# Performance work log

Hardware: AMD Instinct MI355X
Metric: run time of the kernel (lower is better)

The kernel has to match this reference:

```python
import jax, jax.numpy as jnp
import numpy as np

B, T, K = 32, 8192, 16
EPS = 1e-7
LAM_FIRE, LAM_CANCEL, LAM_VALID, LAM_WRITE = 1.0, 1.0, 0.5, 0.5


def setup_inputs() -> dict:
    key = jax.random.key(0)
    ks = jax.random.split(key, 11)
    return {
        "trigger_hazard": jax.random.uniform(ks[0], (B, T, K), jnp.float32),
        "validity": jax.random.uniform(ks[1], (B, T, K), jnp.float32),
        "cancel_logits": jax.random.normal(ks[2], (B, T, K, 3), jnp.float32),
        "write_score": jax.random.normal(ks[3], (B, T, 1), jnp.float32),
        "live_mask": jax.random.randint(ks[4], (B, T, K), 0, 2).astype(bool),
        "contract_id": jax.random.randint(ks[5], (B, T, K), 0, 32),
        "oracle_fire": jax.random.randint(ks[6], (B, T, K), 0, 2).astype(jnp.float32),
        "oracle_cancel": jax.random.randint(ks[7], (B, T, K), 0, 4),
        "oracle_valid": jax.random.randint(ks[8], (B, T, K), 0, 2).astype(jnp.float32),
        "oracle_should_write": jax.random.randint(ks[9], (B, T, 1), 0, 2).astype(jnp.float32),
        "oracle_contract_id": jax.random.randint(ks[10], (B, T, K), 0, 32),
    }


def _masked_bce(p_raw, y, m):
    # Mirrors torch: BCE(clamp(p)*mask, y*mask), then *mask, sum / clamp(mask.sum(),1)
    n = jnp.maximum(m.sum(), 1.0)
    p = jnp.clip(p_raw, EPS, 1.0 - EPS) * m
    t = y * m
    # extra inner clip only guards masked entries (p==0), which are zeroed anyway
    bce = -(t * jnp.log(jnp.clip(p, EPS)) + (1.0 - t) * jnp.log(jnp.clip(1.0 - p, EPS)))
    return (bce * m).sum() / n


def _cancel_ce(logits, cancel_tgt, live_mask):
    has = ((cancel_tgt > 0) & live_mask).astype(jnp.float32)  # (B,T,K)
    n = has.sum()
    tgt = jnp.clip(cancel_tgt - 1, 0).astype(jnp.int32)
    logp = jax.nn.log_softmax(logits, axis=-1)  # (B,T,K,3)
    ce = -jnp.take_along_axis(logp, tgt[..., None], axis=-1)[..., 0]
    return jnp.where(n > 0, (ce * has).sum() / jnp.maximum(n, 1.0), 0.0)


def _bce_with_logits(x, y):
    return jnp.mean(jnp.maximum(x, 0.0) - x * y + jnp.log1p(jnp.exp(-jnp.abs(x))))


def reference(trigger_hazard, validity, cancel_logits, write_score, live_mask,
              contract_id, oracle_fire, oracle_cancel, oracle_valid,
              oracle_should_write, oracle_contract_id):
    # Vectorized align_oracle_to_model: broadcast compare + first-match argmax + gather
    match = (contract_id[..., :, None] == oracle_contract_id[..., None, :]) \
            & (contract_id != 0)[..., None]              # (B,T,Km,Ko)
    found = match.any(axis=-1)                           # (B,T,Km)
    idx = jnp.argmax(match, axis=-1)                     # first matching oracle slot

    def align_f(x):  # float tensors -> zeros where unmatched (torch out = zeros float)
        return jnp.where(found, jnp.take_along_axis(x, idx, axis=2), 0.0)

    fire_t = align_f(oracle_fire)
    valid_t = align_f(oracle_valid)
    cancel_t = jnp.where(found, jnp.take_along_axis(oracle_cancel, idx, axis=2), 0)

    m = live_mask.astype(jnp.float32)
    fire = LAM_FIRE * _masked_bce(trigger_hazard, fire_t, m)
    cancel = LAM_CANCEL * _cancel_ce(cancel_logits, cancel_t, live_mask)
    valid = LAM_VALID * _masked_bce(validity, valid_t, m)
    write = LAM_WRITE * _bce_with_logits(write_score, oracle_should_write)
    total = fire + cancel + valid + write
    return jnp.stack([fire, cancel, valid, write, total])
```

## Files before the change

### kernel.cpp

```cpp
#include <hip/hip_runtime.h>
#include <math.h>

#define EPS_F 1e-7f

constexpr int Bc = 32, Tc = 8192, Kc = 16;
constexpr int ROWS  = Bc * Tc;
constexpr int BLOCK = 256;
constexpr int NBLK  = ROWS / BLOCK;

__global__ __launch_bounds__(BLOCK) void loss_main(
    const float* __restrict__ trig,
    const float* __restrict__ valp,
    const float* __restrict__ clog,
    const float* __restrict__ wscore,
    const int*   __restrict__ live,
    const int*   __restrict__ cid,
    const float* __restrict__ ofire,
    const int*   __restrict__ ocan,
    const float* __restrict__ ovalid,
    const float* __restrict__ oshw,
    const int*   __restrict__ ocid,
    float* __restrict__ part)
{
  const int row = blockIdx.x * BLOCK + threadIdx.x;

  const int4*   ocid4 = (const int4*)  ocid  + row * 4;
  const int4*   ocan4 = (const int4*)  ocan  + row * 4;
  const float4* ofr4  = (const float4*)ofire + row * 4;
  const float4* ovl4  = (const float4*)ovalid+ row * 4;
  const int4*   cid4  = (const int4*)  cid   + row * 4;
  const int4*   liv4  = (const int4*)  live  + row * 4;
  const float4* trg4  = (const float4*)trig  + row * 4;
  const float4* vlp4  = (const float4*)valp  + row * 4;
  const float4* clg4  = (const float4*)clog  + row * 12;

  unsigned found32 = 0u;
  unsigned long long tblLo = 0ull, tblHi = 0ull;
  #pragma unroll
  for (int ch = 0; ch < 4; ++ch) {
    const int4   oc = ocid4[ch];
    const int4   cc = ocan4[ch];
    const float4 ff = ofr4[ch];
    const float4 vv = ovl4[ch];
    const int ocs[4] = {oc.x, oc.y, oc.z, oc.w};
    const int ccs[4] = {cc.x, cc.y, cc.z, cc.w};
    const float ffs[4] = {ff.x, ff.y, ff.z, ff.w};
    const float vvs[4] = {vv.x, vv.y, vv.z, vv.w};
    #pragma unroll
    for (int j = 0; j < 4; ++j) {
      const unsigned c   = (unsigned)ocs[j] & 31u;
      const unsigned nib = (unsigned)ffs[j] | ((unsigned)vvs[j] << 1) |
                           ((unsigned)ccs[j] << 2);
      const unsigned upd = ((found32 >> c) & 1u) ^ 1u;
      const unsigned long long val =
          (unsigned long long)(nib * upd) << ((c & 15u) * 4u);
      tblLo |= (c < 16u) ? val : 0ull;
      tblHi |= (c < 16u) ? 0ull : val;
      found32 |= 1u << c;
    }
  }

  float s0 = 0.f, s1 = 0.f, s2 = 0.f, s3 = 0.f, s4 = 0.f;
  #pragma unroll
  for (int ch = 0; ch < 4; ++ch) {
    const int4   cd = cid4[ch];
    const int4   lm = liv4[ch];
    const float4 ph = trg4[ch];
    const float4 pv = vlp4[ch];
    const float4 lA = clg4[ch * 3 + 0];
    const float4 lB = clg4[ch * 3 + 1];
    const float4 lC = clg4[ch * 3 + 2];
    const int   cds[4] = {cd.x, cd.y, cd.z, cd.w};
    const int   lms[4] = {lm.x, lm.y, lm.z, lm.w};
    const float phs[4] = {ph.x, ph.y, ph.z, ph.w};
    const float pvs[4] = {pv.x, pv.y, pv.z, pv.w};
    const float L0[4] = {lA.x, lA.w, lB.z, lC.y};
    const float L1[4] = {lA.y, lB.x, lB.w, lC.z};
    const float L2[4] = {lA.z, lB.y, lC.x, lC.w};
    #pragma unroll
    for (int j = 0; j < 4; ++j) {
      const unsigned c = (unsigned)cds[j];
      const bool fnd = (c != 0u) && ((found32 >> c) & 1u);
      const unsigned long long sel = (c < 16u) ? tblLo : tblHi;
      unsigned nib = (unsigned)(sel >> ((c & 15u) * 4u)) & 15u;
      nib = fnd ? nib : 0u;
      const float fire_t = (float)(nib & 1u);
      const float val_t  = (float)((nib >> 1) & 1u);
      const int   can_t  = (int)(nib >> 2);

      const float m = lms[j] ? 1.f : 0.f;

      const float p  = fminf(fmaxf(phs[j], EPS_F), 1.f - EPS_F);
      const float bf = -__logf((fire_t != 0.f) ? p : 1.f - p);
      const float q  = fminf(fmaxf(pvs[j], EPS_F), 1.f - EPS_F);
      const float bv = -__logf((val_t != 0.f) ? q : 1.f - q);

      const float has = (can_t > 0 && lms[j]) ? 1.f : 0.f;
      const int tgt = (can_t - 1) < 0 ? 0 : (can_t - 1);
      const float l0 = L0[j], l1 = L1[j], l2 = L2[j];
      const float mx  = fmaxf(l0, fmaxf(l1, l2));
      const float lse = mx + __logf(__expf(l0 - mx) + __expf(l1 - mx) +
                                    __expf(l2 - mx));
      const float lt  = (tgt == 0) ? l0 : ((tgt == 1) ? l1 : l2);

      s0 += bf * m;
      s1 += m;
      s2 += (lse - lt) * has;
      s3 += has;
      s4 += bv * m;
    }
  }

  const float x = wscore[row];
  const float y = oshw[row];
  const float s5 = fmaxf(x, 0.f) - x * y + __logf(1.f + __expf(-fabsf(x)));

  float v[6] = {s0, s1, s2, s3, s4, s5};
  #pragma unroll
  for (int off = 32; off > 0; off >>= 1) {
    #pragma unroll
    for (int i = 0; i < 6; ++i) v[i] += __shfl_down(v[i], off, 64);
  }
  __shared__ float red[4][6];
  const int w = threadIdx.x >> 6, lane = threadIdx.x & 63;
  if (lane == 0) {
    #pragma unroll
    for (int i = 0; i < 6; ++i) red[w][i] = v[i];
  }
  __syncthreads();
  if (threadIdx.x == 0) {
    #pragma unroll
    for (int i = 0; i < 6; ++i)
      part[blockIdx.x * 6 + i] = red[0][i] + red[1][i] + red[2][i] + red[3][i];
  }
}

__global__ __launch_bounds__(BLOCK) void loss_finalize(
    const float* __restrict__ part, float* __restrict__ out)
{
  double v[6] = {0, 0, 0, 0, 0, 0};
  for (int r = threadIdx.x; r < NBLK; r += BLOCK) {
    #pragma unroll
    for (int i = 0; i < 6; ++i) v[i] += (double)part[r * 6 + i];
  }
  #pragma unroll
  for (int off = 32; off > 0; off >>= 1) {
    #pragma unroll
    for (int i = 0; i < 6; ++i) v[i] += __shfl_down(v[i], off, 64);
  }
  __shared__ double red[4][6];
  const int w = threadIdx.x >> 6, lane = threadIdx.x & 63;
  if (lane == 0) {
    #pragma unroll
    for (int i = 0; i < 6; ++i) red[w][i] = v[i];
  }
  __syncthreads();
  if (threadIdx.x == 0) {
    double a[6];
    #pragma unroll
    for (int i = 0; i < 6; ++i) a[i] = red[0][i] + red[1][i] + red[2][i] + red[3][i];
    const double live_n = a[1] < 1.0 ? 1.0 : a[1];
    const double fire   = a[0] / live_n;
    const double cancel = (a[3] > 0.0) ? a[2] / (a[3] < 1.0 ? 1.0 : a[3])
                                       : 0.0;
    const double valid  = 0.5 * a[4] / live_n;
    const double wr     = 0.5 * a[5] / (double)ROWS;
    out[0] = (float)fire;
    out[1] = (float)cancel;
    out[2] = (float)valid;
    out[3] = (float)wr;
    out[4] = (float)(fire + cancel + valid + wr);
  }
}

extern "C" void kernel_launch(void* const* d_in, const int* in_sizes, int n_in,
                              void* d_out, int out_size, void* d_ws, size_t ws_size,
                              hipStream_t stream) {
  const float* trig   = (const float*)d_in[0];
  const float* valp   = (const float*)d_in[1];
  const float* clog   = (const float*)d_in[2];
  const float* wscore = (const float*)d_in[3];
  const int*   live   = (const int*)  d_in[4];
  const int*   cid    = (const int*)  d_in[5];
  const float* ofire  = (const float*)d_in[6];
  const int*   ocan   = (const int*)  d_in[7];
  const float* ovalid = (const float*)d_in[8];
  const float* oshw   = (const float*)d_in[9];
  const int*   ocid   = (const int*)  d_in[10];
  float* out  = (float*)d_out;
  float* part = (float*)d_ws;

  loss_main<<<NBLK, BLOCK, 0, stream>>>(trig, valp, clog, wscore, live, cid,
                                        ofire, ocan, ovalid, oshw, ocid, part);
  loss_finalize<<<1, BLOCK, 0, stream>>>(part, out);
}
```

Baseline: 218.1 us.

## Split each row across four lanes and merge alignment tables via xor shuffles

```diff
diff --git a/kernel.cpp b/kernel.cpp
--- a/kernel.cpp
+++ b/kernel.cpp
@@ -6,7 +6,16 @@
 constexpr int Bc = 32, Tc = 8192, Kc = 16;
 constexpr int ROWS  = Bc * Tc;
 constexpr int BLOCK = 256;
-constexpr int NBLK  = ROWS / BLOCK;
+constexpr int ROWS_PER_BLK = BLOCK / 4;
+constexpr int NBLK  = ROWS / ROWS_PER_BLK;
+
+typedef unsigned long long u64;
+
+__device__ __forceinline__ u64 shflx64(u64 v, int m) {
+  unsigned lo = __shfl_xor((unsigned)v, m, 64);
+  unsigned hi = __shfl_xor((unsigned)(v >> 32), m, 64);
+  return ((u64)hi << 32) | lo;
+}
 
 __global__ __launch_bounds__(BLOCK) void loss_main(
     const float* __restrict__ trig,
@@ -22,67 +31,85 @@
     const int*   __restrict__ ocid,
     float* __restrict__ part)
 {
-  const int row = blockIdx.x * BLOCK + threadIdx.x;
-
-  const int4*   ocid4 = (const int4*)  ocid  + row * 4;
-  const int4*   ocan4 = (const int4*)  ocan  + row * 4;
-  const float4* ofr4  = (const float4*)ofire + row * 4;
-  const float4* ovl4  = (const float4*)ovalid+ row * 4;
-  const int4*   cid4  = (const int4*)  cid   + row * 4;
-  const int4*   liv4  = (const int4*)  live  + row * 4;
-  const float4* trg4  = (const float4*)trig  + row * 4;
-  const float4* vlp4  = (const float4*)valp  + row * 4;
-  const float4* clg4  = (const float4*)clog  + row * 12;
-
-  unsigned found32 = 0u;
-  unsigned long long tblLo = 0ull, tblHi = 0ull;
-  #pragma unroll
-  for (int ch = 0; ch < 4; ++ch) {
-    const int4   oc = ocid4[ch];
-    const int4   cc = ocan4[ch];
-    const float4 ff = ofr4[ch];
-    const float4 vv = ovl4[ch];
-    const int ocs[4] = {oc.x, oc.y, oc.z, oc.w};
-    const int ccs[4] = {cc.x, cc.y, cc.z, cc.w};
+  const int t    = blockIdx.x * BLOCK + threadIdx.x;
+  const int lane = threadIdx.x & 63;
+
+  const int4   oc = ((const int4*)  ocid)[t];
+  const int4   cc = ((const int4*)  ocan)[t];
+  const float4 ff = ((const float4*)ofire)[t];
+  const float4 vv = ((const float4*)ovalid)[t];
+  const int4   cd = ((const int4*)  cid)[t];
+  const int4   lm = ((const int4*)  live)[t];
+  const float4 ph = ((const float4*)trig)[t];
+  const float4 pq = ((const float4*)valp)[t];
+  const float4 lA = ((const float4*)clog)[t * 3 + 0];
+  const float4 lB = ((const float4*)clog)[t * 3 + 1];
+  const float4 lC = ((const float4*)clog)[t * 3 + 2];
+  float ws_x = 0.f, ws_y = 0.f;
+  if (threadIdx.x < ROWS_PER_BLK) {
+    const int r2 = blockIdx.x * ROWS_PER_BLK + threadIdx.x;
+    ws_x = wscore[r2];
+    ws_y = oshw[r2];
+  }
+
+  u64 tblLo = 0ull, tblHi = 0ull, fndLo = 0ull, fndHi = 0ull;
+  {
+    const int   ocs[4] = {oc.x, oc.y, oc.z, oc.w};
+    const int   ccs[4] = {cc.x, cc.y, cc.z, cc.w};
     const float ffs[4] = {ff.x, ff.y, ff.z, ff.w};
     const float vvs[4] = {vv.x, vv.y, vv.z, vv.w};
     #pragma unroll
     for (int j = 0; j < 4; ++j) {
-      const unsigned c   = (unsigned)ocs[j] & 31u;
+      const unsigned c  = (unsigned)ocs[j] & 31u;
+      const unsigned sh = (c & 15u) * 4u;
+      const bool isLo   = c < 16u;
+      const u64 fsel    = isLo ? fndLo : fndHi;
+      const bool seen   = ((fsel >> sh) & 1ull) != 0ull;
       const unsigned nib = (unsigned)ffs[j] | ((unsigned)vvs[j] << 1) |
                            ((unsigned)ccs[j] << 2);
-      const unsigned upd = ((found32 >> c) & 1u) ^ 1u;
-      const unsigned long long val =
-          (unsigned long long)(nib * upd) << ((c & 15u) * 4u);
-      tblLo |= (c < 16u) ? val : 0ull;
-      tblHi |= (c < 16u) ? 0ull : val;
-      found32 |= 1u << c;
+      const u64 add  = seen ? 0ull : ((u64)nib << sh);
+      const u64 fadd = 0xFull << sh;
+      tblLo |= isLo ? add : 0ull;
+      tblHi |= isLo ? 0ull : add;
+      fndLo |= isLo ? fadd : 0ull;
+      fndHi |= isLo ? 0ull : fadd;
     }
   }
 
+  #pragma unroll
+  for (int m = 1; m <= 2; m <<= 1) {
+    const u64 pTL = shflx64(tblLo, m);
+    const u64 pTH = shflx64(tblHi, m);
+    const u64 pFL = shflx64(fndLo, m);
+    const u64 pFH = shflx64(fndHi, m);
+    const bool iLow = (lane & m) == 0;
+    const u64 loTL = iLow ? tblLo : pTL, hiTL = iLow ? pTL : tblLo;
+    const u64 loTH = iLow ? tblHi : pTH, hiTH = iLow ? pTH : tblHi;
+    const u64 loFL = iLow ? fndLo : pFL, hiFL = iLow ? pFL : fndLo;
+    const u64 loFH = iLow ? fndHi : pFH, hiFH = iLow ? pFH : fndHi;
+    tblLo = loTL | (hiTL & ~loFL);
+    tblHi = loTH | (hiTH & ~loFH);
+    fndLo = loFL | hiFL;
+    fndHi = loFH | hiFH;
+  }
+
   float s0 = 0.f, s1 = 0.f, s2 = 0.f, s3 = 0.f, s4 = 0.f;
-  #pragma unroll
-  for (int ch = 0; ch < 4; ++ch) {
-    const int4   cd = cid4[ch];
-    const int4   lm = liv4[ch];
-    const float4 ph = trg4[ch];
-    const float4 pv = vlp4[ch];
-    const float4 lA = clg4[ch * 3 + 0];
-    const float4 lB = clg4[ch * 3 + 1];
-    const float4 lC = clg4[ch * 3 + 2];
+  {
     const int   cds[4] = {cd.x, cd.y, cd.z, cd.w};
     const int   lms[4] = {lm.x, lm.y, lm.z, lm.w};
     const float phs[4] = {ph.x, ph.y, ph.z, ph.w};
-    const float pvs[4] = {pv.x, pv.y, pv.z, pv.w};
+    const float pqs[4] = {pq.x, pq.y, pq.z, pq.w};
     const float L0[4] = {lA.x, lA.w, lB.z, lC.y};
     const float L1[4] = {lA.y, lB.x, lB.w, lC.z};
     const float L2[4] = {lA.z, lB.y, lC.x, lC.w};
     #pragma unroll
     for (int j = 0; j < 4; ++j) {
-      const unsigned c = (unsigned)cds[j];
-      const bool fnd = (c != 0u) && ((found32 >> c) & 1u);
-      const unsigned long long sel = (c < 16u) ? tblLo : tblHi;
-      unsigned nib = (unsigned)(sel >> ((c & 15u) * 4u)) & 15u;
+      const unsigned c  = (unsigned)cds[j] & 31u;
+      const unsigned sh = (c & 15u) * 4u;
+      const bool isLo   = c < 16u;
+      const bool fnd = (c != 0u) &&
+                       ((((isLo ? fndLo : fndHi) >> sh) & 1ull) != 0ull);
+      unsigned nib = (unsigned)(((isLo ? tblLo : tblHi) >> sh)) & 15u;
       nib = fnd ? nib : 0u;
       const float fire_t = (float)(nib & 1u);
       const float val_t  = (float)((nib >> 1) & 1u);
@@ -92,7 +119,7 @@
 
       const float p  = fminf(fmaxf(phs[j], EPS_F), 1.f - EPS_F);
       const float bf = -__logf((fire_t != 0.f) ? p : 1.f - p);
-      const float q  = fminf(fmaxf(pvs[j], EPS_F), 1.f - EPS_F);
+      const float q  = fminf(fmaxf(pqs[j], EPS_F), 1.f - EPS_F);
       const float bv = -__logf((val_t != 0.f) ? q : 1.f - q);
 
       const float has = (can_t > 0 && lms[j]) ? 1.f : 0.f;
@@ -111,9 +138,10 @@
     }
   }
 
-  const float x = wscore[row];
-  const float y = oshw[row];
-  const float s5 = fmaxf(x, 0.f) - x * y + __logf(1.f + __expf(-fabsf(x)));
+  float s5 = 0.f;
+  if (threadIdx.x < ROWS_PER_BLK) {
+    s5 = fmaxf(ws_x, 0.f) - ws_x * ws_y + __logf(1.f + __expf(-fabsf(ws_x)));
+  }
 
   float v[6] = {s0, s1, s2, s3, s4, s5};
   #pragma unroll
@@ -122,7 +150,7 @@
     for (int i = 0; i < 6; ++i) v[i] += __shfl_down(v[i], off, 64);
   }
   __shared__ float red[4][6];
-  const int w = threadIdx.x >> 6, lane = threadIdx.x & 63;
+  const int w = threadIdx.x >> 6;
   if (lane == 0) {
     #pragma unroll
     for (int i = 0; i < 6; ++i) red[w][i] = v[i];
```

New measurement: 214.2 us. No clear change (-1.8%).
